# Optimization experiments

Hardware: AMD Instinct MI355X
Metric: run time of the kernel (lower is better)

## Reference

```python
import jax, jax.numpy as jnp
import numpy as np

NUM_HEADS = 16

def rotate_half(x):
    x1, x2 = jnp.split(x, 2, axis=-1)
    return jnp.concatenate([-x2, x1], axis=-1)

def setup_inputs() -> dict:
    key = jax.random.key(0)
    ks = jax.random.split(key, 12)
    B, S, D = 2, 2048, 1024
    sc = 1.0 / np.sqrt(D)
    return {
        "x": jax.random.normal(ks[0], (B, S, D), dtype=jnp.float32),
        "cdr_mask": jax.random.uniform(ks[1], (B, 1, S, S), dtype=jnp.float32),
        "Wq": jax.random.normal(ks[2], (D, D), dtype=jnp.float32) * sc,
        "bq": jnp.zeros((D,), dtype=jnp.float32),
        "Wk": jax.random.normal(ks[3], (D, D), dtype=jnp.float32) * sc,
        "bk": jnp.zeros((D,), dtype=jnp.float32),
        "Wv": jax.random.normal(ks[4], (D, D), dtype=jnp.float32) * sc,
        "bv": jnp.zeros((D,), dtype=jnp.float32),
        "Wo": jax.random.normal(ks[5], (D, D), dtype=jnp.float32) * sc,
        "bo": jnp.zeros((D,), dtype=jnp.float32),
        "cdr_weight": jnp.asarray(1.0, dtype=jnp.float32),
    }

def reference(x, cdr_mask, Wq, bq, Wk, bk, Wv, bv, Wo, bo, cdr_weight):
    B, S, D = x.shape
    H = NUM_HEADS
    hd = D // H
    # RoPE tables: NOTE original uses full head_dim frequencies (not head_dim/2)
    inv_freq = 1.0 / (10000.0 ** (jnp.arange(hd, dtype=jnp.float32) / hd))
    pos = jnp.arange(S, dtype=jnp.float32)
    sinusoid = pos[:, None] * inv_freq[None, :]          # [S, hd]
    sin_pos = jnp.sin(sinusoid)[None, None]              # [1,1,S,hd]
    cos_pos = jnp.cos(sinusoid)[None, None]

    def heads(y):  # [B,S,D] -> [B,H,S,hd]
        return y.reshape(B, S, H, hd).transpose(0, 2, 1, 3)

    Q = heads(x @ Wq + bq)
    K = heads(x @ Wk + bk)
    V = heads(x @ Wv + bv)
    Qr = Q * cos_pos + rotate_half(Q) * sin_pos
    Kr = K * cos_pos + rotate_half(K) * sin_pos

    scores = jnp.einsum('bhqd,bhkd->bhqk', Qr, Kr) / jnp.sqrt(jnp.asarray(hd, x.dtype))
    scores = scores * (1.0 + cdr_mask * cdr_weight)      # multiplicative learned mask
    attn = jax.nn.softmax(scores, axis=-1)               # dropout is identity in eval
    out = jnp.einsum('bhqk,bhkd->bhqd', attn, V)
    out = out.transpose(0, 2, 1, 3).reshape(B, S, D)
    return out @ Wo + bo
```

## Files before the change

### kernel.cpp

```cpp
#include <hip/hip_runtime.h>
#include <stdint.h>

typedef unsigned short u16;
typedef __bf16 bf16x8 __attribute__((ext_vector_type(8)));
typedef float f32x4 __attribute__((ext_vector_type(4)));
typedef float fx4 __attribute__((ext_vector_type(4)));
typedef unsigned short u16x8 __attribute__((ext_vector_type(8)));
typedef unsigned short u16x4 __attribute__((ext_vector_type(4)));

#define DEV __device__ __forceinline__

DEV u16 f2bf(float f) {
  unsigned u = __builtin_bit_cast(unsigned, f);
  u += 0x7fff + ((u >> 16) & 1);
  return (u16)(u >> 16);
}

DEV f32x4 mfma16(bf16x8 a, bf16x8 b, f32x4 c) {
  return __builtin_amdgcn_mfma_f32_16x16x32_bf16(a, b, c, 0, 0, 0);
}

DEV void gload16(const void* g, void* l) {
  __builtin_amdgcn_global_load_lds(
      (const __attribute__((address_space(1))) unsigned int*)g,
      (__attribute__((address_space(3))) unsigned int*)l, 16, 0, 0);
}

__global__ __launch_bounds__(256) void k_tables(float* __restrict__ cosT,
                                                float* __restrict__ sinT) {
  int i = blockIdx.x * 256 + threadIdx.x;
  int s = i >> 6, d = i & 63;
  float inv = exp2f(-(float)d * (13.287712379549449f / 64.f));
  float a = (float)s * inv;
  cosT[i] = cosf(a);
  sinT[i] = sinf(a);
}

__global__ __launch_bounds__(256) void k_cvt(const float* __restrict__ x,
                                             u16* __restrict__ xb) {
  int i = (blockIdx.x * 256 + threadIdx.x) * 4;
  fx4 f = *reinterpret_cast<const fx4*>(x + i);
  u16x4 o;
#pragma unroll
  for (int j = 0; j < 4; ++j) o[j] = f2bf(f[j]);
  *reinterpret_cast<u16x4*>(xb + i) = o;
}

__global__ __launch_bounds__(256) void k_wtrans(
    const float* __restrict__ W0, const float* __restrict__ W1,
    const float* __restrict__ W2, const float* __restrict__ W3,
    u16* __restrict__ O0, u16* __restrict__ O1,
    u16* __restrict__ O2, u16* __restrict__ O3) {
  __shared__ u16 T[64][66];
  const float* W = (blockIdx.z == 0) ? W0 : (blockIdx.z == 1) ? W1
                   : (blockIdx.z == 2) ? W2 : W3;
  u16* O = (blockIdx.z == 0) ? O0 : (blockIdx.z == 1) ? O1
           : (blockIdx.z == 2) ? O2 : O3;
  const int t = threadIdx.x;
  const int k0 = blockIdx.y * 64, n0 = blockIdx.x * 64;
  const int r = t >> 2, cc = (t & 3) * 16;
  const float* src = W + (long)(k0 + r) * 1024 + n0 + cc;
#pragma unroll
  for (int u = 0; u < 16; u += 4) {
    fx4 f = *reinterpret_cast<const fx4*>(src + u);
#pragma unroll
    for (int j = 0; j < 4; ++j) T[r][cc + u + j] = f2bf(f[j]);
  }
  __syncthreads();
  const int n = t >> 2, kc = (t & 3) * 16;
  u16x8 o1, o2;
#pragma unroll
  for (int j = 0; j < 8; ++j) { o1[j] = T[kc + j][n]; o2[j] = T[kc + 8 + j][n]; }
  u16* dst = O + (long)(n0 + n) * 1024 + k0 + kc;
  *reinterpret_cast<u16x8*>(dst) = o1;
  *reinterpret_cast<u16x8*>(dst + 8) = o2;
}

__global__ __launch_bounds__(256) void k_gemm_qkv(
    const u16* __restrict__ A, const u16* __restrict__ Bt,
    const float* __restrict__ bq, const float* __restrict__ bk,
    const float* __restrict__ bv, const float* __restrict__ cosT,
    const float* __restrict__ sinT, u16* __restrict__ qb,
    u16* __restrict__ kb, u16* __restrict__ vb) {
  __shared__ u16 As[128 * 32];
  __shared__ u16 Bs[128 * 32];
  const int t = threadIdx.x;
  const int lane = t & 63, wid = t >> 6;
  const int wm = wid >> 1, wn = wid & 1;
  const int l15 = lane & 15, lg = lane >> 4;
  const int bm = blockIdx.x, bn = blockIdx.y;

  f32x4 acc[4][4];
#pragma unroll
  for (int m = 0; m < 4; ++m)
#pragma unroll
    for (int n = 0; n < 4; ++n) acc[m][n] = f32x4{0.f, 0.f, 0.f, 0.f};

  const int arow = t >> 2;
  const int acol = (t & 3) << 3;
  const u16* Ab = A + (long)(bm * 128 + arow) * 1024 + acol;
  const u16* Bb = Bt + (long)(bn * 128 + arow) * 1024 + acol;

  for (int k0 = 0; k0 < 1024; k0 += 32) {
    gload16(Ab + k0, As + t * 8);
    gload16(Ab + 64 * 1024 + k0, As + 2048 + t * 8);
    gload16(Bb + k0, Bs + t * 8);
    gload16(Bb + 64 * 1024 + k0, Bs + 2048 + t * 8);
    __syncthreads();
    bf16x8 af[4], bfr[4];
#pragma unroll
    for (int m = 0; m < 4; ++m)
      af[m] = *reinterpret_cast<const bf16x8*>(As + (wm * 64 + m * 16 + l15) * 32 + lg * 8);
#pragma unroll
    for (int n = 0; n < 4; ++n)
      bfr[n] = *reinterpret_cast<const bf16x8*>(Bs + (wn * 64 + n * 16 + l15) * 32 + lg * 8);
#pragma unroll
    for (int m = 0; m < 4; ++m)
#pragma unroll
      for (int n = 0; n < 4; ++n) acc[m][n] = mfma16(af[m], bfr[n], acc[m][n]);
    __syncthreads();
  }

  const int seg = bn >> 3;
  const float* bias = (seg == 0) ? bq : (seg == 1) ? bk : bv;
  u16* outb = (seg == 0) ? qb : (seg == 1) ? kb : vb;
  const int h = (bn & 7) * 2 + wn;
#pragma unroll
  for (int m = 0; m < 4; ++m) {
#pragma unroll
    for (int reg = 0; reg < 4; ++reg) {
      const int rg = bm * 128 + wm * 64 + m * 16 + lg * 4 + reg;
      const int s = rg & 2047, b = rg >> 11;
      float v4[4];
#pragma unroll
      for (int n = 0; n < 4; ++n)
        v4[n] = acc[m][n][reg] + bias[(bn & 7) * 128 + wn * 64 + n * 16 + l15];
      if (seg < 2) {
#pragma unroll
        for (int n = 0; n < 4; ++n) {
          const int d = n * 16 + l15;
          float c = cosT[s * 64 + d], sn = sinT[s * 64 + d];
          float rot = (n < 2) ? -v4[n + 2] : v4[n - 2];
          outb[((long)(b * 16 + h) * 2048 + s) * 64 + d] = f2bf(v4[n] * c + rot * sn);
        }
      } else {
#pragma unroll
        for (int n = 0; n < 4; ++n)
          outb[((long)(b * 16 + h) * 2048 + s) * 64 + n * 16 + l15] = f2bf(v4[n]);
      }
    }
  }
}

__global__ __launch_bounds__(256) void k_gemm_out(
    const u16* __restrict__ A, const u16* __restrict__ Bt,
    const float* __restrict__ bias, float* __restrict__ outf) {
  __shared__ u16 As[128 * 32];
  __shared__ u16 Bs[128 * 32];
  const int t = threadIdx.x;
  const int lane = t & 63, wid = t >> 6;
  const int wm = wid >> 1, wn = wid & 1;
  const int l15 = lane & 15, lg = lane >> 4;
  const int bm = blockIdx.x, bn = blockIdx.y;

  f32x4 acc[4][4];
#pragma unroll
  for (int m = 0; m < 4; ++m)
#pragma unroll
    for (int n = 0; n < 4; ++n) acc[m][n] = f32x4{0.f, 0.f, 0.f, 0.f};

  const int arow = t >> 2;
  const int acol = (t & 3) << 3;
  const u16* Ab = A + (long)(bm * 128 + arow) * 1024 + acol;
  const u16* Bb = Bt + (long)(bn * 128 + arow) * 1024 + acol;

  for (int k0 = 0; k0 < 1024; k0 += 32) {
    gload16(Ab + k0, As + t * 8);
    gload16(Ab + 64 * 1024 + k0, As + 2048 + t * 8);
    gload16(Bb + k0, Bs + t * 8);
    gload16(Bb + 64 * 1024 + k0, Bs + 2048 + t * 8);
    __syncthreads();
    bf16x8 af[4], bfr[4];
#pragma unroll
    for (int m = 0; m < 4; ++m)
      af[m] = *reinterpret_cast<const bf16x8*>(As + (wm * 64 + m * 16 + l15) * 32 + lg * 8);
#pragma unroll
    for (int n = 0; n < 4; ++n)
      bfr[n] = *reinterpret_cast<const bf16x8*>(Bs + (wn * 64 + n * 16 + l15) * 32 + lg * 8);
#pragma unroll
    for (int m = 0; m < 4; ++m)
#pragma unroll
      for (int n = 0; n < 4; ++n) acc[m][n] = mfma16(af[m], bfr[n], acc[m][n]);
    __syncthreads();
  }

#pragma unroll
  for (int m = 0; m < 4; ++m)
#pragma unroll
    for (int reg = 0; reg < 4; ++reg) {
      const int rg = bm * 128 + wm * 64 + m * 16 + lg * 4 + reg;
#pragma unroll
      for (int n = 0; n < 4; ++n)
        outf[(long)rg * 1024 + bn * 128 + wn * 64 + n * 16 + l15] =
            acc[m][n][reg] + bias[bn * 128 + wn * 64 + n * 16 + l15];
    }
}

__global__ __launch_bounds__(256) void k_vtrans(const u16* __restrict__ VB,
                                                u16* __restrict__ VT) {
  __shared__ u16 T[64][66];
  const int t = threadIdx.x;
  const int bh = blockIdx.y;
  const int s0 = blockIdx.x * 64;
  const int r = t >> 2, c = (t & 3) * 16;
  const u16* src = VB + ((long)bh * 2048 + s0 + r) * 64 + c;
  u16x8 a = *reinterpret_cast<const u16x8*>(src);
  u16x8 b = *reinterpret_cast<const u16x8*>(src + 8);
#pragma unroll
  for (int j = 0; j < 8; ++j) { T[r][c + j] = a[j]; T[r][c + 8 + j] = b[j]; }
  __syncthreads();
  const int d = t >> 2, sc = (t & 3) * 16;
  u16x8 o1, o2;
#pragma unroll
  for (int j = 0; j < 8; ++j) { o1[j] = T[sc + j][d]; o2[j] = T[sc + 8 + j][d]; }
  u16* dst = VT + ((long)bh * 64 + d) * 2048 + s0 + sc;
  *reinterpret_cast<u16x8*>(dst) = o1;
  *reinterpret_cast<u16x8*>(dst + 8) = o2;
}

__global__ __launch_bounds__(256, 4) void k_attn(
    const u16* __restrict__ Qb, const u16* __restrict__ Kb,
    const u16* __restrict__ Vt, const float* __restrict__ mask,
    const float* __restrict__ wp, u16* __restrict__ Ob) {
  __shared__ u16 Ks[2][64 * 64];
  __shared__ u16 Vs[2][64 * 64];
  __shared__ u16 Ps[4][16 * 64];
  const int t = threadIdx.x, lane = t & 63, wid = t >> 6;
  const int l15 = lane & 15, lg = lane >> 4;
  const int b = blockIdx.z, hh = blockIdx.y;
  const int bh = b * 16 + hh;
  const int qw = blockIdx.x * 64 + wid * 16;
  const float c1 = 0.18033688f;
  const float c2 = c1 * wp[0];

  bf16x8 qf[2];
  const u16* Qrow = Qb + ((long)bh * 2048 + qw + l15) * 64 + lg * 8;
  qf[0] = *reinterpret_cast<const bf16x8*>(Qrow);
  qf[1] = *reinterpret_cast<const bf16x8*>(Qrow + 32);

  bf16x8 ones;
#pragma unroll
  for (int j = 0; j < 8; ++j) ones[j] = (__bf16)1.0f;

  f32x4 oacc[4];
#pragma unroll
  for (int n = 0; n < 4; ++n) oacc[n] = f32x4{0.f, 0.f, 0.f, 0.f};
  f32x4 lsum = f32x4{0.f, 0.f, 0.f, 0.f};

  const u16* Kbase = Kb + (long)bh * 2048 * 64;
  const u16* Vbase = Vt + (long)bh * 64 * 2048;
  const float* Mbase = mask + (long)b * 2048 * 2048 + (long)(qw + lg * 4) * 2048 + l15;

  const int krow = t >> 3;
  const int kcs = ((t & 7) * 8) ^ ((krow & 7) << 3);

#define STAGE(buf, kt)                                                       \
  do {                                                                       \
    gload16(Kbase + (long)((kt) + krow) * 64 + kcs, Ks[buf] + t * 8);        \
    gload16(Kbase + (long)((kt) + krow + 32) * 64 + kcs,                     \
            Ks[buf] + 2048 + t * 8);                                         \
    gload16(Vbase + (long)krow * 2048 + (kt) + kcs, Vs[buf] + t * 8);        \
    gload16(Vbase + (long)(krow + 32) * 2048 + (kt) + kcs,                   \
            Vs[buf] + 2048 + t * 8);                                         \
  } while (0)

  STAGE(0, 0);
  __syncthreads();
  int cur = 0;

  for (int kt = 0; kt < 2048; kt += 64) {
    if (kt + 64 < 2048) STAGE(cur ^ 1, kt + 64);

    float mv[4][4];
#pragma unroll
    for (int reg = 0; reg < 4; ++reg)
#pragma unroll
      for (int n = 0; n < 4; ++n)
        mv[reg][n] = Mbase[(long)reg * 2048 + kt + n * 16];

    f32x4 sc[4];
#pragma unroll
    for (int n = 0; n < 4; ++n) sc[n] = f32x4{0.f, 0.f, 0.f, 0.f};
#pragma unroll
    for (int ks = 0; ks < 2; ++ks) {
      const int ko = (ks * 32 + lg * 8) ^ ((l15 & 7) << 3);
#pragma unroll
      for (int n = 0; n < 4; ++n) {
        bf16x8 kf = *reinterpret_cast<const bf16x8*>(Ks[cur] + (n * 16 + l15) * 64 + ko);
        sc[n] = mfma16(qf[ks], kf, sc[n]);
      }
    }

#pragma unroll
    for (int n = 0; n < 4; ++n)
#pragma unroll
      for (int reg = 0; reg < 4; ++reg) {
        float mult = __builtin_fmaf(mv[reg][n], c2, c1);
        float p = exp2f(sc[n][reg] * mult);
        const int r = lg * 4 + reg;
        Ps[wid][r * 64 + ((n * 16 + l15) ^ ((r & 7) << 3))] =
            __builtin_bit_cast(u16, (__bf16)p);
      }

#pragma unroll
    for (int ks = 0; ks < 2; ++ks) {
      const int ko = (ks * 32 + lg * 8) ^ ((l15 & 7) << 3);
      bf16x8 pf = *reinterpret_cast<const bf16x8*>(Ps[wid] + l15 * 64 + ko);
      lsum = mfma16(pf, ones, lsum);
#pragma unroll
      for (int n = 0; n < 4; ++n) {
        bf16x8 vf = *reinterpret_cast<const bf16x8*>(Vs[cur] + (n * 16 + l15) * 64 + ko);
        oacc[n] = mfma16(pf, vf, oacc[n]);
      }
    }
    __syncthreads();
    cur ^= 1;
  }
#undef STAGE

#pragma unroll
  for (int n = 0; n < 4; ++n)
#pragma unroll
    for (int reg = 0; reg < 4; ++reg) {
      float v = oacc[n][reg] / lsum[reg];
      Ob[((long)b * 2048 + qw + lg * 4 + reg) * 1024 + hh * 64 + n * 16 + l15] = f2bf(v);
    }
}

extern "C" void kernel_launch(void* const* d_in, const int* in_sizes, int n_in,
                              void* d_out, int out_size, void* d_ws, size_t ws_size,
                              hipStream_t stream) {
  const float* x  = (const float*)d_in[0];
  const float* cm = (const float*)d_in[1];
  const float* Wq = (const float*)d_in[2];
  const float* bq = (const float*)d_in[3];
  const float* Wk = (const float*)d_in[4];
  const float* bk = (const float*)d_in[5];
  const float* Wv = (const float*)d_in[6];
  const float* bv = (const float*)d_in[7];
  const float* Wo = (const float*)d_in[8];
  const float* bo = (const float*)d_in[9];
  const float* cw = (const float*)d_in[10];
  float* out = (float*)d_out;

  char* ws = (char*)d_ws;
  float* cosT = (float*)(ws + 0);
  float* sinT = (float*)(ws + (512u << 10));
  u16* xb  = (u16*)(ws + (1u << 20));
  u16* wqT = (u16*)(ws + (9u << 20));
  u16* woT = (u16*)(ws + (15u << 20));
  u16* qb  = (u16*)(ws + (17u << 20));
  u16* kb  = (u16*)(ws + (25u << 20));
  u16* vb  = (u16*)(ws + (33u << 20));
  u16* vt  = (u16*)(ws + (41u << 20));
  u16* ob  = (u16*)(ws + (49u << 20));
  u16* wkT = wqT + (1u << 20);
  u16* wvT = wqT + (2u << 20);

  k_tables<<<512, 256, 0, stream>>>(cosT, sinT);
  k_cvt<<<4096, 256, 0, stream>>>(x, xb);
  k_wtrans<<<dim3(16, 16, 4), 256, 0, stream>>>(Wq, Wk, Wv, Wo, wqT, wkT, wvT, woT);
  k_gemm_qkv<<<dim3(32, 24), 256, 0, stream>>>(xb, wqT, bq, bk, bv, cosT, sinT, qb, kb, vb);
  k_vtrans<<<dim3(32, 32), 256, 0, stream>>>(vb, vt);
  k_attn<<<dim3(32, 16, 2), 256, 0, stream>>>(qb, kb, vt, cm, cw, ob);
  k_gemm_out<<<dim3(32, 8), 256, 0, stream>>>(ob, woT, bo, out);
}
```

Baseline: 257.2 us.

## Process 32 query rows per wave in attention to reuse K/V tiles

```diff
diff --git a/kernel.cpp b/kernel.cpp
--- a/kernel.cpp
+++ b/kernel.cpp
@@ -228,34 +228,39 @@
   *reinterpret_cast<u16x8*>(dst + 8) = o2;
 }
 
-__global__ __launch_bounds__(256, 4) void k_attn(
+__global__ __launch_bounds__(256, 2) void k_attn(
     const u16* __restrict__ Qb, const u16* __restrict__ Kb,
     const u16* __restrict__ Vt, const float* __restrict__ mask,
     const float* __restrict__ wp, u16* __restrict__ Ob) {
   __shared__ u16 Ks[2][64 * 64];
   __shared__ u16 Vs[2][64 * 64];
-  __shared__ u16 Ps[4][16 * 64];
+  __shared__ u16 Ps[4][32 * 64];
   const int t = threadIdx.x, lane = t & 63, wid = t >> 6;
   const int l15 = lane & 15, lg = lane >> 4;
   const int b = blockIdx.z, hh = blockIdx.y;
   const int bh = b * 16 + hh;
-  const int qw = blockIdx.x * 64 + wid * 16;
+  const int qw = blockIdx.x * 128 + wid * 32;
   const float c1 = 0.18033688f;
   const float c2 = c1 * wp[0];
 
-  bf16x8 qf[2];
-  const u16* Qrow = Qb + ((long)bh * 2048 + qw + l15) * 64 + lg * 8;
-  qf[0] = *reinterpret_cast<const bf16x8*>(Qrow);
-  qf[1] = *reinterpret_cast<const bf16x8*>(Qrow + 32);
+  bf16x8 qf[2][2];
+#pragma unroll
+  for (int m = 0; m < 2; ++m) {
+    const u16* Qrow = Qb + ((long)bh * 2048 + qw + m * 16 + l15) * 64 + lg * 8;
+    qf[m][0] = *reinterpret_cast<const bf16x8*>(Qrow);
+    qf[m][1] = *reinterpret_cast<const bf16x8*>(Qrow + 32);
+  }
 
   bf16x8 ones;
 #pragma unroll
   for (int j = 0; j < 8; ++j) ones[j] = (__bf16)1.0f;
 
-  f32x4 oacc[4];
-#pragma unroll
-  for (int n = 0; n < 4; ++n) oacc[n] = f32x4{0.f, 0.f, 0.f, 0.f};
-  f32x4 lsum = f32x4{0.f, 0.f, 0.f, 0.f};
+  f32x4 oacc[2][4];
+#pragma unroll
+  for (int m = 0; m < 2; ++m)
+#pragma unroll
+    for (int n = 0; n < 4; ++n) oacc[m][n] = f32x4{0.f, 0.f, 0.f, 0.f};
+  f32x4 lsum[2] = {f32x4{0.f, 0.f, 0.f, 0.f}, f32x4{0.f, 0.f, 0.f, 0.f}};
 
   const u16* Kbase = Kb + (long)bh * 2048 * 64;
   const u16* Vbase = Vt + (long)bh * 64 * 2048;
@@ -281,60 +286,76 @@
   for (int kt = 0; kt < 2048; kt += 64) {
     if (kt + 64 < 2048) STAGE(cur ^ 1, kt + 64);
 
-    float mv[4][4];
-#pragma unroll
-    for (int reg = 0; reg < 4; ++reg)
-#pragma unroll
-      for (int n = 0; n < 4; ++n)
-        mv[reg][n] = Mbase[(long)reg * 2048 + kt + n * 16];
-
-    f32x4 sc[4];
-#pragma unroll
-    for (int n = 0; n < 4; ++n) sc[n] = f32x4{0.f, 0.f, 0.f, 0.f};
+    float mv[2][4][4];
+#pragma unroll
+    for (int m = 0; m < 2; ++m)
+#pragma unroll
+      for (int reg = 0; reg < 4; ++reg)
+#pragma unroll
+        for (int n = 0; n < 4; ++n)
+          mv[m][reg][n] = Mbase[(long)(m * 16 + reg) * 2048 + kt + n * 16];
+
+    f32x4 sc[2][4];
+#pragma unroll
+    for (int m = 0; m < 2; ++m)
+#pragma unroll
+      for (int n = 0; n < 4; ++n) sc[m][n] = f32x4{0.f, 0.f, 0.f, 0.f};
 #pragma unroll
     for (int ks = 0; ks < 2; ++ks) {
       const int ko = (ks * 32 + lg * 8) ^ ((l15 & 7) << 3);
+      bf16x8 kf[4];
+#pragma unroll
+      for (int n = 0; n < 4; ++n)
+        kf[n] = *reinterpret_cast<const bf16x8*>(Ks[cur] + (n * 16 + l15) * 64 + ko);
+#pragma unroll
+      for (int m = 0; m < 2; ++m)
+#pragma unroll
+        for (int n = 0; n < 4; ++n) sc[m][n] = mfma16(qf[m][ks], kf[n], sc[m][n]);
+    }
+
+#pragma unroll
+    for (int m = 0; m < 2; ++m)
+#pragma unroll
+      for (int n = 0; n < 4; ++n)
+#pragma unroll
+        for (int reg = 0; reg < 4; ++reg) {
+          float mult = __builtin_fmaf(mv[m][reg][n], c2, c1);
+          float p = exp2f(sc[m][n][reg] * mult);
+          const int r = m * 16 + lg * 4 + reg;
+          Ps[wid][r * 64 + ((n * 16 + l15) ^ ((r & 7) << 3))] =
+              __builtin_bit_cast(u16, (__bf16)p);
+        }
+
+#pragma unroll
+    for (int ks = 0; ks < 2; ++ks) {
+      const int ko = (ks * 32 + lg * 8) ^ ((l15 & 7) << 3);
+      bf16x8 pf[2];
+      pf[0] = *reinterpret_cast<const bf16x8*>(Ps[wid] + l15 * 64 + ko);
+      pf[1] = *reinterpret_cast<const bf16x8*>(Ps[wid] + (16 + l15) * 64 + ko);
+      lsum[0] = mfma16(pf[0], ones, lsum[0]);
+      lsum[1] = mfma16(pf[1], ones, lsum[1]);
 #pragma unroll
       for (int n = 0; n < 4; ++n) {
-        bf16x8 kf = *reinterpret_cast<const bf16x8*>(Ks[cur] + (n * 16 + l15) * 64 + ko);
-        sc[n] = mfma16(qf[ks], kf, sc[n]);
+        bf16x8 vf = *reinterpret_cast<const bf16x8*>(Vs[cur] + (n * 16 + l15) * 64 + ko);
+        oacc[0][n] = mfma16(pf[0], vf, oacc[0][n]);
+        oacc[1][n] = mfma16(pf[1], vf, oacc[1][n]);
       }
     }
-
+    __syncthreads();
+    cur ^= 1;
+  }
+#undef STAGE
+
+#pragma unroll
+  for (int m = 0; m < 2; ++m)
 #pragma unroll
     for (int n = 0; n < 4; ++n)
 #pragma unroll
       for (int reg = 0; reg < 4; ++reg) {
-        float mult = __builtin_fmaf(mv[reg][n], c2, c1);
-        float p = exp2f(sc[n][reg] * mult);
-        const int r = lg * 4 + reg;
-        Ps[wid][r * 64 + ((n * 16 + l15) ^ ((r & 7) << 3))] =
-            __builtin_bit_cast(u16, (__bf16)p);
+        float v = oacc[m][n][reg] / lsum[m][reg];
+        Ob[((long)b * 2048 + qw + m * 16 + lg * 4 + reg) * 1024 + hh * 64 + n * 16 + l15] =
+            f2bf(v);
       }
-
-#pragma unroll
-    for (int ks = 0; ks < 2; ++ks) {
-      const int ko = (ks * 32 + lg * 8) ^ ((l15 & 7) << 3);
-      bf16x8 pf = *reinterpret_cast<const bf16x8*>(Ps[wid] + l15 * 64 + ko);
-      lsum = mfma16(pf, ones, lsum);
-#pragma unroll
-      for (int n = 0; n < 4; ++n) {
-        bf16x8 vf = *reinterpret_cast<const bf16x8*>(Vs[cur] + (n * 16 + l15) * 64 + ko);
-        oacc[n] = mfma16(pf, vf, oacc[n]);
-      }
-    }
-    __syncthreads();
-    cur ^= 1;
-  }
-#undef STAGE
-
-#pragma unroll
-  for (int n = 0; n < 4; ++n)
-#pragma unroll
-    for (int reg = 0; reg < 4; ++reg) {
-      float v = oacc[n][reg] / lsum[reg];
-      Ob[((long)b * 2048 + qw + lg * 4 + reg) * 1024 + hh * 64 + n * 16 + l15] = f2bf(v);
-    }
 }
 
 extern "C" void kernel_launch(void* const* d_in, const int* in_sizes, int n_in,
@@ -372,6 +393,6 @@
   k_wtrans<<<dim3(16, 16, 4), 256, 0, stream>>>(Wq, Wk, Wv, Wo, wqT, wkT, wvT, woT);
   k_gemm_qkv<<<dim3(32, 24), 256, 0, stream>>>(xb, wqT, bq, bk, bv, cosT, sinT, qb, kb, vb);
   k_vtrans<<<dim3(32, 32), 256, 0, stream>>>(vb, vt);
-  k_attn<<<dim3(32, 16, 2), 256, 0, stream>>>(qb, kb, vt, cm, cw, ob);
+  k_attn<<<dim3(16, 16, 2), 256, 0, stream>>>(qb, kb, vt, cm, cw, ob);
   k_gemm_out<<<dim3(32, 8), 256, 0, stream>>>(ob, woT, bo, out);
 }
```

After: 262.8 us. +2.2%, slower.
